# Kernel optimization log

Measured on AMD Instinct MI355X. Metric: run time of the kernel, lower is better.

Reference implementation:

```python
import jax, jax.numpy as jnp
import numpy as np

INPUT_DIM = 2048
N_EXPERTS = 64
K = 2


def setup_inputs() -> dict:
    key = jax.random.key(0)
    kx, kw, kb = jax.random.split(key, 3)
    x = jax.random.normal(kx, (4, 4096, INPUT_DIM), dtype=jnp.float32)
    # nn.Linear(input_dim, n_experts): weight [n_experts, input_dim], bias [n_experts]
    bound = 1.0 / np.sqrt(INPUT_DIM)
    W = jax.random.uniform(kw, (N_EXPERTS, INPUT_DIM), minval=-bound, maxval=bound, dtype=jnp.float32)
    b = jax.random.uniform(kb, (N_EXPERTS,), minval=-bound, maxval=bound, dtype=jnp.float32)
    return {"x": x, "W": W, "b": b}


def reference(x, W, b):
    # logits: [B, S, E]
    logits = jnp.einsum('bsd,ed->bse', x, W) + b
    topk_vals, topk_indices = jax.lax.top_k(logits, K)  # over last (expert) axis
    gate_probs = jax.nn.softmax(topk_vals, axis=-1)
    return gate_probs, topk_indices
```

## Files before the change

### kernel.cpp

```cpp
#include <hip/hip_runtime.h>
#include <math.h>
#include <stdint.h>

typedef _Float16 half8 __attribute__((ext_vector_type(8)));
typedef float floatx4 __attribute__((ext_vector_type(4)));

#define NTOK   16384
#define DIM    2048
#define NEXP   64
#define MB     32
#define NBLK   (NTOK / MB)
#define KC     64
#define NCHUNK (DIM / KC)
#define WSW_H8 16384
#define WSW_BYTES (2 * WSW_H8 * 16)

#define A_BYTES 8192
#define B_BYTES 16384
#define AOFF(b) ((b) * A_BYTES)
#define BOFF(b) (3 * A_BYTES + (b) * B_BYTES)
#define SMEM_BYTES (3 * A_BYTES + 3 * B_BYTES)

__global__ void wprep_kernel(const float* __restrict__ W, _Float16* __restrict__ wsw) {
    const int id   = blockIdx.x * blockDim.x + threadIdx.x;
    const int lane = id & 63;
    const int tg   = (id >> 6) & 3;
    const int sg   = id >> 8;
    const int e    = tg * 16 + (lane & 15);
    const int k    = sg * 32 + (lane >> 4) * 8;
    const float* src = W + (size_t)e * DIM + k;
    half8 h, l;
#pragma unroll
    for (int j = 0; j < 8; j++) {
        const float v  = src[j];
        const _Float16 hh = (_Float16)v;
        h[j] = hh;
        l[j] = (_Float16)((v - (float)hh) * 2048.0f);
    }
    const size_t slot = (size_t)(sg * 4 + tg) * 64 + lane;
    ((half8*)wsw)[slot]          = h;
    ((half8*)wsw)[WSW_H8 + slot] = l;
}

__device__ __forceinline__ void split_a(const float4& v0, const float4& v1,
                                        half8& hi, half8& lo) {
    const float av[8] = {v0.x, v0.y, v0.z, v0.w, v1.x, v1.y, v1.z, v1.w};
#pragma unroll
    for (int j = 0; j < 8; j++) {
        const _Float16 hh = (_Float16)av[j];
        hi[j] = hh;
        lo[j] = (_Float16)((av[j] - (float)hh) * 2048.0f);
    }
}

__device__ __forceinline__ void dma16(const void* g, const char* l) {
    __builtin_amdgcn_global_load_lds(
        (const __attribute__((address_space(1))) unsigned int*)(uintptr_t)g,
        (__attribute__((address_space(3))) unsigned int*)(uintptr_t)l,
        16, 0, 0);
}

template <int N>
__device__ __forceinline__ void wait_vm() {
    asm volatile("s_waitcnt vmcnt(%0)" :: "n"(N) : "memory");
}

template <bool USE_WS>
__global__ __launch_bounds__(256, 2)
void gating_lds_kernel(const float* __restrict__ x, const float* __restrict__ W,
                       const _Float16* __restrict__ wsw, const float* __restrict__ bias,
                       float* __restrict__ out)
{
    __shared__ char smem[SMEM_BYTES];

    const int tid  = threadIdx.x;
    const int lane = tid & 63;
    const int w    = tid >> 6;
    const int mt   = w & 1;
    const int nh   = w >> 1;
    const int col  = lane & 15;
    const int quad = lane >> 4;
    const int tok0 = blockIdx.x * MB;
    const int m    = mt * 16 + col;

    const float* gA[2];
    unsigned     lA[2];
#pragma unroll
    for (int i = 0; i < 2; i++) {
        const int a   = w * 2 + i;
        const int row = a * 4 + (lane >> 4);
        const int pz  = lane & 15;
        const int gp  = (pz & 8) | ((pz & 7) ^ (row & 7));
        gA[i] = x + (size_t)(tok0 + row) * DIM + gp * 4;
        lA[i] = (unsigned)(a * 1024);
    }
    const half8* gB[4];
    unsigned     lB[4];
    if constexpr (USE_WS) {
#pragma unroll
        for (int j = 0; j < 4; j++) {
            const int b = w * 4 + j;
            const int split = b >> 3, idx = b & 7;
            gB[j] = (const half8*)wsw + (size_t)split * WSW_H8 + idx * 64 + lane;
            lB[j] = (unsigned)(split * 8192 + idx * 1024);
        }
    }
    constexpr int OPW = USE_WS ? 6 : 2;

    floatx4 accm[2] = {{0,0,0,0},{0,0,0,0}};
    floatx4 accl[2] = {{0,0,0,0},{0,0,0,0}};

#pragma unroll
    for (int c0 = 0; c0 < 2; c0++) {
#pragma unroll
        for (int i = 0; i < 2; i++)
            dma16(gA[i] + (size_t)c0 * KC, smem + AOFF(c0) + lA[i]);
        if constexpr (USE_WS) {
#pragma unroll
            for (int j = 0; j < 4; j++)
                dma16(gB[j] + (size_t)c0 * 512, smem + BOFF(c0) + lB[j]);
        }
    }

    int bi = 0, pi = 2;
    for (int c = 0; c < NCHUNK; ++c) {
        if (c < NCHUNK - 1) wait_vm<OPW>();
        else                wait_vm<0>();
        __builtin_amdgcn_s_barrier();
        asm volatile("" ::: "memory");

        if (c + 2 < NCHUNK) {
#pragma unroll
            for (int i = 0; i < 2; i++)
                dma16(gA[i] + (size_t)(c + 2) * KC, smem + AOFF(pi) + lA[i]);
            if constexpr (USE_WS) {
#pragma unroll
                for (int j = 0; j < 4; j++)
                    dma16(gB[j] + (size_t)(c + 2) * 512, smem + BOFF(pi) + lB[j]);
            }
        }

        const char* Ab = smem + AOFF(bi);
        const char* Bb = smem + BOFF(bi);
#pragma unroll
        for (int s = 0; s < 2; s++) {
            const float4 v0 = *(const float4*)(Ab + m * 256 + (8 * s + ((2 * quad + 0) ^ (m & 7))) * 16);
            const float4 v1 = *(const float4*)(Ab + m * 256 + (8 * s + ((2 * quad + 1) ^ (m & 7))) * 16);
            half8 ah, alo;
            split_a(v0, v1, ah, alo);
#pragma unroll
            for (int t = 0; t < 2; t++) {
                const int tg = nh * 2 + t;
                half8 bh, bl;
                if constexpr (USE_WS) {
                    bh = *(const half8*)(Bb + (s * 4 + tg) * 1024 + lane * 16);
                    bl = *(const half8*)(Bb + 8192 + (s * 4 + tg) * 1024 + lane * 16);
                } else {
                    const float* wr = W + (size_t)(tg * 16 + col) * DIM + c * KC + s * 32 + quad * 8;
                    split_a(*(const float4*)wr, *(const float4*)(wr + 4), bh, bl);
                }
                accm[t] = __builtin_amdgcn_mfma_f32_16x16x32_f16(ah,  bh, accm[t], 0, 0, 0);
                accl[t] = __builtin_amdgcn_mfma_f32_16x16x32_f16(ah,  bl, accl[t], 0, 0, 0);
                accl[t] = __builtin_amdgcn_mfma_f32_16x16x32_f16(alo, bh, accl[t], 0, 0, 0);
            }
        }
        bi = (bi == 2) ? 0 : bi + 1;
        pi = (pi == 2) ? 0 : pi + 1;
    }

    __syncthreads();
    float* lg = (float*)smem;
    const float inv = 1.0f / 2048.0f;
#pragma unroll
    for (int t = 0; t < 2; t++) {
        const int tg = nh * 2 + t;
#pragma unroll
        for (int r = 0; r < 4; r++) {
            lg[(mt * 16 + quad * 4 + r) * 65 + tg * 16 + col] = accm[t][r] + accl[t][r] * inv;
        }
    }
    __syncthreads();

    if (tid < MB) {
        const int t = tid;
        float v0 = -INFINITY, v1 = -INFINITY;
        int   i0 = 0, i1 = 0;
        for (int e = 0; e < NEXP; e++) {
            const float v = lg[t * 65 + e] + bias[e];
            if (v > v0) { v1 = v0; i1 = i0; v0 = v; i0 = e; }
            else if (v > v1) { v1 = v; i1 = e; }
        }
        const float e1 = expf(v1 - v0);
        const float sden = 1.f + e1;
        const int   g  = tok0 + t;
        out[2 * g + 0] = 1.f / sden;
        out[2 * g + 1] = e1 / sden;
        out[2 * NTOK + 2 * g + 0] = (float)i0;
        out[2 * NTOK + 2 * g + 1] = (float)i1;
    }
}

extern "C" void kernel_launch(void* const* d_in, const int* in_sizes, int n_in,
                              void* d_out, int out_size, void* d_ws, size_t ws_size,
                              hipStream_t stream) {
    const float* x    = (const float*)d_in[0];
    const float* W    = (const float*)d_in[1];
    const float* bias = (const float*)d_in[2];
    float*       out  = (float*)d_out;
    _Float16*    wsw  = (_Float16*)d_ws;

    if (ws_size >= (size_t)WSW_BYTES) {
        hipLaunchKernelGGL(wprep_kernel, dim3(64), dim3(256), 0, stream, W, wsw);
        hipLaunchKernelGGL((gating_lds_kernel<true>), dim3(NBLK), dim3(256), 0, stream,
                           x, W, wsw, bias, out);
    } else {
        hipLaunchKernelGGL((gating_lds_kernel<false>), dim3(NBLK), dim3(256), 0, stream,
                           x, W, wsw, bias, out);
    }
}
```

Baseline: 208.6 us.

## Double token tile per block and halve K chunk with 512 threads

Each workgroup now processes 64 tokens with 8 waves instead of 32 tokens with 4 waves, and the K-chunk shrinks from 64 to 32, so each thread issues one A and one B LDS DMA per chunk. The aim is to halve how often the pre-split fp16 weight tiles are re-read per token and to simplify the load addressing. The cost is twice as many chunk iterations, and so twice as many barriers. There are also fewer bytes in flight per CU, since half as many blocks run, which can expose global memory latency.

```diff
diff --git a/kernel.cpp b/kernel.cpp
--- a/kernel.cpp
+++ b/kernel.cpp
@@ -8,15 +8,15 @@
 #define NTOK   16384
 #define DIM    2048
 #define NEXP   64
-#define MB     32
+#define MB     64
 #define NBLK   (NTOK / MB)
-#define KC     64
+#define KC     32
 #define NCHUNK (DIM / KC)
 #define WSW_H8 16384
 #define WSW_BYTES (2 * WSW_H8 * 16)
 
 #define A_BYTES 8192
-#define B_BYTES 16384
+#define B_BYTES 8192
 #define AOFF(b) ((b) * A_BYTES)
 #define BOFF(b) (3 * A_BYTES + (b) * B_BYTES)
 #define SMEM_BYTES (3 * A_BYTES + 3 * B_BYTES)
@@ -66,7 +66,7 @@
 }
 
 template <bool USE_WS>
-__global__ __launch_bounds__(256, 2)
+__global__ __launch_bounds__(512, 2)
 void gating_lds_kernel(const float* __restrict__ x, const float* __restrict__ W,
                        const _Float16* __restrict__ wsw, const float* __restrict__ bias,
                        float* __restrict__ out)
@@ -76,50 +76,35 @@
     const int tid  = threadIdx.x;
     const int lane = tid & 63;
     const int w    = tid >> 6;
-    const int mt   = w & 1;
-    const int nh   = w >> 1;
+    const int mt   = w & 3;
+    const int nh   = w >> 2;
     const int col  = lane & 15;
     const int quad = lane >> 4;
     const int tok0 = blockIdx.x * MB;
     const int m    = mt * 16 + col;
 
-    const float* gA[2];
-    unsigned     lA[2];
-#pragma unroll
-    for (int i = 0; i < 2; i++) {
-        const int a   = w * 2 + i;
-        const int row = a * 4 + (lane >> 4);
-        const int pz  = lane & 15;
-        const int gp  = (pz & 8) | ((pz & 7) ^ (row & 7));
-        gA[i] = x + (size_t)(tok0 + row) * DIM + gp * 4;
-        lA[i] = (unsigned)(a * 1024);
+    const int arow = w * 8 + (lane >> 3);
+    const int apz  = lane & 7;
+    const int agp  = apz ^ (arow & 7);
+    const float* gA = x + (size_t)(tok0 + arow) * DIM + agp * 4;
+    const unsigned lA = (unsigned)(w * 1024);
+    const half8* gB = nullptr;
+    unsigned     lB = 0;
+    if constexpr (USE_WS) {
+        const int split = w >> 2, tg = w & 3;
+        gB = (const half8*)wsw + (size_t)split * WSW_H8 + tg * 64 + lane;
+        lB = (unsigned)(split * 4096 + tg * 1024);
     }
-    const half8* gB[4];
-    unsigned     lB[4];
-    if constexpr (USE_WS) {
-#pragma unroll
-        for (int j = 0; j < 4; j++) {
-            const int b = w * 4 + j;
-            const int split = b >> 3, idx = b & 7;
-            gB[j] = (const half8*)wsw + (size_t)split * WSW_H8 + idx * 64 + lane;
-            lB[j] = (unsigned)(split * 8192 + idx * 1024);
-        }
-    }
-    constexpr int OPW = USE_WS ? 6 : 2;
+    constexpr int OPW = USE_WS ? 2 : 1;
 
     floatx4 accm[2] = {{0,0,0,0},{0,0,0,0}};
     floatx4 accl[2] = {{0,0,0,0},{0,0,0,0}};
 
 #pragma unroll
     for (int c0 = 0; c0 < 2; c0++) {
-#pragma unroll
-        for (int i = 0; i < 2; i++)
-            dma16(gA[i] + (size_t)c0 * KC, smem + AOFF(c0) + lA[i]);
-        if constexpr (USE_WS) {
-#pragma unroll
-            for (int j = 0; j < 4; j++)
-                dma16(gB[j] + (size_t)c0 * 512, smem + BOFF(c0) + lB[j]);
-        }
+        dma16(gA + (size_t)c0 * KC, smem + AOFF(c0) + lA);
+        if constexpr (USE_WS)
+            dma16(gB + (size_t)c0 * 256, smem + BOFF(c0) + lB);
     }
 
     int bi = 0, pi = 2;
@@ -130,39 +115,31 @@
         asm volatile("" ::: "memory");
 
         if (c + 2 < NCHUNK) {
-#pragma unroll
-            for (int i = 0; i < 2; i++)
-                dma16(gA[i] + (size_t)(c + 2) * KC, smem + AOFF(pi) + lA[i]);
-            if constexpr (USE_WS) {
-#pragma unroll
-                for (int j = 0; j < 4; j++)
-                    dma16(gB[j] + (size_t)(c + 2) * 512, smem + BOFF(pi) + lB[j]);
-            }
+            dma16(gA + (size_t)(c + 2) * KC, smem + AOFF(pi) + lA);
+            if constexpr (USE_WS)
+                dma16(gB + (size_t)(c + 2) * 256, smem + BOFF(pi) + lB);
         }
 
         const char* Ab = smem + AOFF(bi);
         const char* Bb = smem + BOFF(bi);
+        const float4 v0 = *(const float4*)(Ab + m * 128 + (((2 * quad + 0) ^ (m & 7))) * 16);
+        const float4 v1 = *(const float4*)(Ab + m * 128 + (((2 * quad + 1) ^ (m & 7))) * 16);
+        half8 ah, alo;
+        split_a(v0, v1, ah, alo);
 #pragma unroll
-        for (int s = 0; s < 2; s++) {
-            const float4 v0 = *(const float4*)(Ab + m * 256 + (8 * s + ((2 * quad + 0) ^ (m & 7))) * 16);
-            const float4 v1 = *(const float4*)(Ab + m * 256 + (8 * s + ((2 * quad + 1) ^ (m & 7))) * 16);
-            half8 ah, alo;
-            split_a(v0, v1, ah, alo);
-#pragma unroll
-            for (int t = 0; t < 2; t++) {
-                const int tg = nh * 2 + t;
-                half8 bh, bl;
-                if constexpr (USE_WS) {
-                    bh = *(const half8*)(Bb + (s * 4 + tg) * 1024 + lane * 16);
-                    bl = *(const half8*)(Bb + 8192 + (s * 4 + tg) * 1024 + lane * 16);
-                } else {
-                    const float* wr = W + (size_t)(tg * 16 + col) * DIM + c * KC + s * 32 + quad * 8;
-                    split_a(*(const float4*)wr, *(const float4*)(wr + 4), bh, bl);
-                }
-                accm[t] = __builtin_amdgcn_mfma_f32_16x16x32_f16(ah,  bh, accm[t], 0, 0, 0);
-                accl[t] = __builtin_amdgcn_mfma_f32_16x16x32_f16(ah,  bl, accl[t], 0, 0, 0);
-                accl[t] = __builtin_amdgcn_mfma_f32_16x16x32_f16(alo, bh, accl[t], 0, 0, 0);
+        for (int t = 0; t < 2; t++) {
+            const int tg = nh * 2 + t;
+            half8 bh, bl;
+            if constexpr (USE_WS) {
+                bh = *(const half8*)(Bb + tg * 1024 + lane * 16);
+                bl = *(const half8*)(Bb + 4096 + tg * 1024 + lane * 16);
+            } else {
+                const float* wr = W + (size_t)(tg * 16 + col) * DIM + c * KC + quad * 8;
+                split_a(*(const float4*)wr, *(const float4*)(wr + 4), bh, bl);
             }
+            accm[t] = __builtin_amdgcn_mfma_f32_16x16x32_f16(ah,  bh, accm[t], 0, 0, 0);
+            accl[t] = __builtin_amdgcn_mfma_f32_16x16x32_f16(ah,  bl, accl[t], 0, 0, 0);
+            accl[t] = __builtin_amdgcn_mfma_f32_16x16x32_f16(alo, bh, accl[t], 0, 0, 0);
         }
         bi = (bi == 2) ? 0 : bi + 1;
         pi = (pi == 2) ? 0 : pi + 1;
@@ -211,10 +188,10 @@
 
     if (ws_size >= (size_t)WSW_BYTES) {
         hipLaunchKernelGGL(wprep_kernel, dim3(64), dim3(256), 0, stream, W, wsw);
-        hipLaunchKernelGGL((gating_lds_kernel<true>), dim3(NBLK), dim3(256), 0, stream,
+        hipLaunchKernelGGL((gating_lds_kernel<true>), dim3(NBLK), dim3(512), 0, stream,
                            x, W, wsw, bias, out);
     } else {
-        hipLaunchKernelGGL((gating_lds_kernel<false>), dim3(NBLK), dim3(256), 0, stream,
+        hipLaunchKernelGGL((gating_lds_kernel<false>), dim3(NBLK), dim3(512), 0, stream,
                            x, W, wsw, bias, out);
     }
 }
```

Result: slower. 226.4 us (+8.6%).
